# Kernel tuning notes

Hardware: AMD Instinct MI355X
Metric: run time of the kernel (lower is better)

The kernel has to match this reference:

```python
import jax, jax.numpy as jnp
import numpy as np

EPS = 1e-10
LN_EPS = 1e-5
NEG = -1e30
H = 8  # attention_head


def _layernorm(x, g, b):
    mu = jnp.mean(x, axis=-1, keepdims=True)
    var = jnp.mean(jnp.square(x - mu), axis=-1, keepdims=True)
    return (x - mu) * jax.lax.rsqrt(var + LN_EPS) * g + b


def setup_inputs() -> dict:
    key = jax.random.key(0)
    ks = jax.random.split(key, 10)
    B, T, D = 4, 1024, 1024
    inputs = jax.random.normal(ks[0], (B, T, D), dtype=jnp.float32)
    lengths = jax.random.randint(ks[1], (B,), T // 2, T + 1).astype(jnp.int32)
    lengths = lengths.at[0].set(T)  # at least one full-length sequence
    noise_u = jax.random.uniform(ks[2], (B, H, T, T), dtype=jnp.float32)
    w = lambda k: (jax.random.normal(k, (D, D), dtype=jnp.float32) * 0.02)
    return {
        'inputs': inputs, 'lengths': lengths, 'noise_u': noise_u,
        'Wq': w(ks[3]), 'Wk': w(ks[4]), 'Wv': w(ks[5]),
        'Weq': w(ks[6]), 'Wek': w(ks[7]), 'Wfc': w(ks[8]),
        'bfc': jnp.zeros((D,), jnp.float32),
        'ln1_g': jnp.ones((D,), jnp.float32), 'ln1_b': jnp.zeros((D,), jnp.float32),
        'ln2_g': jnp.ones((D,), jnp.float32), 'ln2_b': jnp.zeros((D,), jnp.float32),
    }


def reference(inputs, lengths, noise_u, Wq, Wk, Wv, Weq, Wek, Wfc, bfc,
              ln1_g, ln1_b, ln2_g, ln2_b):
    B, T, D = inputs.shape
    dh = D // H
    # length mask: True where padded
    pad = jnp.arange(T)[None, :] >= lengths[:, None]            # (B, T)
    x = jnp.where(pad[:, :, None], 0.0, inputs)                  # zero padded positions

    def heads(W):
        h = x @ W.T                                              # (B,T,D)
        return h.reshape(B, T, H, dh).transpose(0, 2, 1, 3)      # (B,H,T,dh)

    q, k, v, eq, ek = (heads(W) for W in (Wq, Wk, Wv, Weq, Wek))
    scores = jnp.einsum('bhqd,bhkd->bhqk', q, k) / jnp.sqrt(jnp.float32(D))
    edge = jnp.einsum('bhqd,bhkd->bhqk', eq, ek)                 # (B,H,T,T)

    # bernoulli prior: binary-concrete sample (hard threshold), tau=1
    edges_prob = jax.nn.sigmoid(edge)
    logistic = jnp.log(noise_u + EPS) - jnp.log(1.0 - noise_u + EPS)
    y_soft = jax.nn.sigmoid(jnp.log(edges_prob + EPS) - jnp.log(1.0 - edges_prob + EPS) + logistic)
    gate = y_soft > 0.5                                          # hard edges (condition only, as in torch .data)

    valid = gate & (~pad[:, None, None, :])                      # gate AND key-length mask
    s = jnp.where(valid, scores, NEG)
    attn = jax.nn.softmax(s, axis=-1)
    attn = jnp.where(jnp.any(valid, axis=-1, keepdims=True), attn, 0.0)  # nan->0 for fully-masked rows

    ctx = jax.nn.relu(jnp.einsum('bhqk,bhkd->bhqd', attn, v))
    ctx = ctx.transpose(0, 2, 1, 3).reshape(B, T, D)

    h1 = _layernorm(ctx + x, ln1_g, ln1_b)
    h2 = jax.nn.relu(h1 @ Wfc.T + bfc) + h1
    out = _layernorm(h2, ln2_g, ln2_b)
    out = jnp.where(pad[:, :, None], 0.0, out)
    return out, attn, edges_prob
```

## Files before the change

### kernel.cpp

```cpp
#include <hip/hip_runtime.h>
#include <math.h>

constexpr int Bn = 4, Tn = 1024, Dn = 1024, Hn = 8, DH = 128;
constexpr float EPSF = 1e-10f;
constexpr float LN_EPSF = 1e-5f;
constexpr float NEGF = -1e30f;

typedef __attribute__((ext_vector_type(8))) short bf16x8;
typedef __attribute__((ext_vector_type(4))) float f32x4;
typedef __attribute__((ext_vector_type(4))) unsigned uint4v;

#define MFMA16(a, b, c) __builtin_amdgcn_mfma_f32_16x16x32_bf16(a, b, c, 0, 0, 0)

__device__ __forceinline__ short f2bf(float f) {
    unsigned u = __builtin_bit_cast(unsigned, f);
    u += 0x7fffu + ((u >> 16) & 1u);
    return (short)(u >> 16);
}
__device__ __forceinline__ float bf2f(short h) {
    return __builtin_bit_cast(float, ((unsigned)(unsigned short)h) << 16);
}
__device__ __forceinline__ unsigned pack2(float a, float b) {
    return ((unsigned)(unsigned short)f2bf(a)) | (((unsigned)(unsigned short)f2bf(b)) << 16);
}

__device__ __forceinline__ void gload16(const void* g, void* l) {
    __builtin_amdgcn_global_load_lds((__attribute__((address_space(1))) void*)g,
                                     (__attribute__((address_space(3))) void*)l,
                                     16, 0, 0);
}

template <int NW>
__device__ __forceinline__ void stage_b(const short* g, int ld, short* lds, int lane, int wid) {
#pragma unroll
    for (int s = 0; s < 8 / NW; ++s) {
        const int ii = wid * (8 / NW) + s;
        const int c = ii * 64 + lane;
        const int kb = c >> 7, r = c & 127;
        gload16(g + (size_t)r * ld + kb * 8, lds + ii * 512);
    }
}

template <int NW>
__device__ __forceinline__ void stage_f(const float* g, int ld, float* lds, int lane, int wid) {
#pragma unroll
    for (int s = 0; s < 16 / NW; ++s) {
        const int ii = wid * (16 / NW) + s;
        const int c = ii * 64 + lane;
        const int kb = c >> 8, half = (c >> 7) & 1, r = c & 127;
        gload16(g + (size_t)r * ld + kb * 8 + half * 4, lds + ii * 256);
    }
}

__device__ __forceinline__ bf16x8 fragb(const short* lds, int kbl, int r) {
    return *reinterpret_cast<const bf16x8*>(lds + kbl * 1024 + r * 8);
}

__device__ __forceinline__ bf16x8 fragf(const float* lds, int kbl, int r) {
    const f32x4 lo = *reinterpret_cast<const f32x4*>(lds + kbl * 1024 + r * 4);
    const f32x4 hi = *reinterpret_cast<const f32x4*>(lds + kbl * 1024 + 512 + r * 4);
    uint4v p;
    p[0] = pack2(lo[0], lo[1]);
    p[1] = pack2(lo[2], lo[3]);
    p[2] = pack2(hi[0], hi[1]);
    p[3] = pack2(hi[2], hi[3]);
    return __builtin_bit_cast(bf16x8, p);
}

struct CvtP { const float* src[6]; short* hi; short* lo; };

__global__ __launch_bounds__(256) void cvt_w(CvtP p) {
    const int i = blockIdx.x * 256 + threadIdx.x;
    const int mat = i >> 17;
    const int off = (i & 131071) * 8;
    const float* s = p.src[mat] + off;
    const float4 a = *reinterpret_cast<const float4*>(s);
    const float4 b = *reinterpret_cast<const float4*>(s + 4);
    const float va[8] = {a.x, a.y, a.z, a.w, b.x, b.y, b.z, b.w};
    bf16x8 h, l;
#pragma unroll
    for (int j = 0; j < 8; ++j) {
        h[j] = f2bf(va[j]);
        l[j] = f2bf(va[j] - bf2f(h[j]));
    }
    *reinterpret_cast<bf16x8*>(p.hi + (size_t)mat * 1048576 + off) = h;
    if (mat >= 3)
        *reinterpret_cast<bf16x8*>(p.lo + (size_t)(mat - 3) * 1048576 + off) = l;
}

__global__ __launch_bounds__(256) void mask_x(const float4* __restrict__ in,
                                              const int* __restrict__ lengths,
                                              short* __restrict__ xhi,
                                              short* __restrict__ xlo) {
    const int i = blockIdx.x * 256 + threadIdx.x;
    const int row = i >> 8;
    const int t = row & 1023, b = row >> 10;
    float4 v = in[i];
    if (t >= lengths[b]) { v.x = 0.f; v.y = 0.f; v.z = 0.f; v.w = 0.f; }
    short4 h, l;
    h.x = f2bf(v.x); h.y = f2bf(v.y); h.z = f2bf(v.z); h.w = f2bf(v.w);
    l.x = f2bf(v.x - bf2f(h.x)); l.y = f2bf(v.y - bf2f(h.y));
    l.z = f2bf(v.z - bf2f(h.z)); l.w = f2bf(v.w - bf2f(h.w));
    *reinterpret_cast<short4*>(xhi + (size_t)i * 4) = h;
    *reinterpret_cast<short4*>(xlo + (size_t)i * 4) = l;
}

struct ProjP { const short* whi[5]; const short* wlo[2]; short* o[5]; short* olo[2]; };

__global__ __launch_bounds__(256) void proj_mfma(const short* __restrict__ Xh,
                                                 const short* __restrict__ Xl, ProjP p) {
    __shared__ alignas(16) short T0[4096];
    __shared__ alignas(16) short T1[4096];
    __shared__ alignas(16) short T2[4096];
    __shared__ alignas(16) short T3[4096];
    const int z = blockIdx.z;
    const short* __restrict__ Wh = p.whi[z];
    const int m0 = blockIdx.y << 7, n0 = blockIdx.x << 7;
    const int tid = threadIdx.x, lane = tid & 63, wid = tid >> 6;
    const int wm = (wid >> 1) << 6, wn = (wid & 1) << 6;
    const int kbl = lane >> 4, rl = lane & 15, rw = (lane >> 4) << 2;
    f32x4 acc[4][4] = {};
    if (z < 3) {
        for (int k0 = 0; k0 < Dn; k0 += 32) {
            stage_b<4>(Xh + (size_t)m0 * Dn + k0, Dn, T0, lane, wid);
            stage_b<4>(Wh + (size_t)n0 * Dn + k0, Dn, T1, lane, wid);
            __syncthreads();
            bf16x8 a[4], b[4];
#pragma unroll
            for (int f = 0; f < 4; ++f) {
                a[f] = fragb(T0, kbl, wm + f * 16 + rl);
                b[f] = fragb(T1, kbl, wn + f * 16 + rl);
            }
#pragma unroll
            for (int i = 0; i < 4; ++i)
#pragma unroll
                for (int j = 0; j < 4; ++j)
                    acc[i][j] = MFMA16(a[i], b[j], acc[i][j]);
            __syncthreads();
        }
    } else {
        const short* __restrict__ Wl = p.wlo[z - 3];
        for (int k0 = 0; k0 < Dn; k0 += 32) {
            stage_b<4>(Xh + (size_t)m0 * Dn + k0, Dn, T0, lane, wid);
            stage_b<4>(Xl + (size_t)m0 * Dn + k0, Dn, T1, lane, wid);
            stage_b<4>(Wh + (size_t)n0 * Dn + k0, Dn, T2, lane, wid);
            stage_b<4>(Wl + (size_t)n0 * Dn + k0, Dn, T3, lane, wid);
            __syncthreads();
            bf16x8 ah[4], al[4], bh[4], bl[4];
#pragma unroll
            for (int f = 0; f < 4; ++f) {
                ah[f] = fragb(T0, kbl, wm + f * 16 + rl);
                al[f] = fragb(T1, kbl, wm + f * 16 + rl);
                bh[f] = fragb(T2, kbl, wn + f * 16 + rl);
                bl[f] = fragb(T3, kbl, wn + f * 16 + rl);
            }
#pragma unroll
            for (int i = 0; i < 4; ++i)
#pragma unroll
                for (int j = 0; j < 4; ++j) {
                    acc[i][j] = MFMA16(al[i], bh[j], acc[i][j]);
                    acc[i][j] = MFMA16(ah[i], bl[j], acc[i][j]);
                    acc[i][j] = MFMA16(ah[i], bh[j], acc[i][j]);
                }
            __syncthreads();
        }
    }
    short* __restrict__ O = p.o[z];
    short* __restrict__ OL = (z >= 3) ? p.olo[z - 3] : nullptr;
#pragma unroll
    for (int i = 0; i < 4; ++i)
#pragma unroll
        for (int r = 0; r < 4; ++r) {
            const int m = m0 + wm + i * 16 + rw + r;
            const int b = m >> 10, t = m & 1023;
#pragma unroll
            for (int j = 0; j < 4; ++j) {
                const int n = n0 + wn + j * 16 + rl;
                const int h = n >> 7, d = n & 127;
                const float av = acc[i][j][r];
                if (z == 2) {
                    O[(((size_t)(b * Hn + h) * DH + d) << 10) + t] = f2bf(av);
                } else {
                    const size_t idx = (((size_t)(b * Hn + h)) << 10 | t) * DH + d;
                    const short hi = f2bf(av);
                    O[idx] = hi;
                    if (z >= 3) OL[idx] = f2bf(av - bf2f(hi));
                }
            }
        }
}

__global__ __launch_bounds__(256) void scores_edge(
    const short* __restrict__ Q, const short* __restrict__ Kb,
    const short* __restrict__ EQh, const short* __restrict__ EQl,
    const short* __restrict__ EKh, const short* __restrict__ EKl,
    const float* __restrict__ U, const int* __restrict__ lens,
    float* __restrict__ S, float* __restrict__ EP) {
    __shared__ alignas(16) short T0[4096];
    __shared__ alignas(16) short T1[4096];
    __shared__ alignas(16) short T2[4096];
    __shared__ alignas(16) short T3[4096];
    const int z = blockIdx.z;
    const int len = lens[z >> 3];
    const int m0 = blockIdx.y << 7, n0 = blockIdx.x << 7;
    const int tid = threadIdx.x, lane = tid & 63, wid = tid >> 6;
    const int wm = (wid >> 1) << 6, wn = (wid & 1) << 6;
    const int kbl = lane >> 4, rl = lane & 15, rw = (lane >> 4) << 2;
    const size_t zo = (size_t)z << 17;

    f32x4 acce[4][4] = {};
    for (int k0 = 0; k0 < DH; k0 += 32) {
        stage_b<4>(EQh + zo + (size_t)m0 * DH + k0, DH, T0, lane, wid);
        stage_b<4>(EQl + zo + (size_t)m0 * DH + k0, DH, T1, lane, wid);
        stage_b<4>(EKh + zo + (size_t)n0 * DH + k0, DH, T2, lane, wid);
        stage_b<4>(EKl + zo + (size_t)n0 * DH + k0, DH, T3, lane, wid);
        __syncthreads();
        bf16x8 ah[4], al[4], bh[4], bl[4];
#pragma unroll
        for (int f = 0; f < 4; ++f) {
            ah[f] = fragb(T0, kbl, wm + f * 16 + rl);
            al[f] = fragb(T1, kbl, wm + f * 16 + rl);
            bh[f] = fragb(T2, kbl, wn + f * 16 + rl);
            bl[f] = fragb(T3, kbl, wn + f * 16 + rl);
        }
#pragma unroll
        for (int i = 0; i < 4; ++i)
#pragma unroll
            for (int j = 0; j < 4; ++j) {
                acce[i][j] = MFMA16(al[i], bl[j], acce[i][j]);
                acce[i][j] = MFMA16(al[i], bh[j], acce[i][j]);
                acce[i][j] = MFMA16(ah[i], bl[j], acce[i][j]);
                acce[i][j] = MFMA16(ah[i], bh[j], acce[i][j]);
            }
        __syncthreads();
    }

    f32x4 accs[4][4] = {};
    for (int k0 = 0; k0 < DH; k0 += 32) {
        stage_b<4>(Q + zo + (size_t)m0 * DH + k0, DH, T0, lane, wid);
        stage_b<4>(Kb + zo + (size_t)n0 * DH + k0, DH, T1, lane, wid);
        __syncthreads();
        bf16x8 a[4], b[4];
#pragma unroll
        for (int f = 0; f < 4; ++f) {
            a[f] = fragb(T0, kbl, wm + f * 16 + rl);
            b[f] = fragb(T1, kbl, wn + f * 16 + rl);
        }
#pragma unroll
        for (int i = 0; i < 4; ++i)
#pragma unroll
            for (int j = 0; j < 4; ++j)
                accs[i][j] = MFMA16(a[i], b[j], accs[i][j]);
        __syncthreads();
    }

#pragma unroll
    for (int i = 0; i < 4; ++i)
#pragma unroll
        for (int r = 0; r < 4; ++r) {
            const int m = m0 + wm + i * 16 + rw + r;
#pragma unroll
            for (int j = 0; j < 4; ++j) {
                const int n = n0 + wn + j * 16 + rl;
                const size_t idx = ((size_t)z << 20) + ((size_t)m << 10) + n;
                const float e = acce[i][j][r];
                const float pp = 1.f / (1.f + expf(-e));
                EP[idx] = pp;
                const float u = U[idx];
                const float zz = logf(pp + EPSF) - logf(1.f - pp + EPSF) +
                                 logf(u + EPSF) - logf(1.f - u + EPSF);
                const bool valid = (zz > 0.f) && (n < len);
                S[idx] = valid ? accs[i][j][r] * (1.f / 32.f) : NEGF;
            }
        }
}

__global__ __launch_bounds__(256) void softmax_rows(float* __restrict__ attn) {
    __shared__ float redm[4];
    __shared__ float reds[4];
    const size_t base = (size_t)blockIdx.x * Tn;
    float4* rowp = reinterpret_cast<float4*>(attn + base);
    float4 s = rowp[threadIdx.x];
    float m = fmaxf(fmaxf(s.x, s.y), fmaxf(s.z, s.w));
#pragma unroll
    for (int off = 32; off >= 1; off >>= 1) m = fmaxf(m, __shfl_xor(m, off));
    if ((threadIdx.x & 63) == 0) redm[threadIdx.x >> 6] = m;
    __syncthreads();
    m = fmaxf(fmaxf(redm[0], redm[1]), fmaxf(redm[2], redm[3]));
    const bool any = m > -5e29f;
    float4 e;
    e.x = expf(s.x - m); e.y = expf(s.y - m);
    e.z = expf(s.z - m); e.w = expf(s.w - m);
    float sum = e.x + e.y + e.z + e.w;
#pragma unroll
    for (int off = 32; off >= 1; off >>= 1) sum += __shfl_xor(sum, off);
    if ((threadIdx.x & 63) == 0) reds[threadIdx.x >> 6] = sum;
    __syncthreads();
    sum = reds[0] + reds[1] + reds[2] + reds[3];
    const float inv = any ? 1.f / sum : 0.f;
    e.x *= inv; e.y *= inv; e.z *= inv; e.w *= inv;
    rowp[threadIdx.x] = e;
}

__global__ __launch_bounds__(512) void ctx_mfma(const float* __restrict__ P,
                                                const short* __restrict__ Vt,
                                                float* __restrict__ C) {
    __shared__ alignas(16) float Ps[4096];
    __shared__ alignas(16) short Vs[4096];
    const int z = blockIdx.y;
    const int bb = z >> 3, h = z & 7;
    const int m0 = blockIdx.x << 7;
    const int tid = threadIdx.x, lane = tid & 63, wid = tid >> 6;
    const int wm = (wid >> 2) << 6, wn = (wid & 3) << 5;
    const int kbl = lane >> 4, rl = lane & 15, rw = (lane >> 4) << 2;
    f32x4 acc[4][2] = {};
    for (int k0 = 0; k0 < Tn; k0 += 32) {
        stage_f<8>(P + ((size_t)z << 20) + ((size_t)m0 << 10) + k0, Tn, Ps, lane, wid);
        stage_b<8>(Vt + ((size_t)z << 17) + k0, Tn, Vs, lane, wid);
        __syncthreads();
        bf16x8 a[4], b[2];
#pragma unroll
        for (int f = 0; f < 4; ++f) a[f] = fragf(Ps, kbl, wm + f * 16 + rl);
#pragma unroll
        for (int f = 0; f < 2; ++f) b[f] = fragb(Vs, kbl, wn + f * 16 + rl);
#pragma unroll
        for (int i = 0; i < 4; ++i)
#pragma unroll
            for (int j = 0; j < 2; ++j)
                acc[i][j] = MFMA16(a[i], b[j], acc[i][j]);
        __syncthreads();
    }
#pragma unroll
    for (int i = 0; i < 4; ++i)
#pragma unroll
        for (int r = 0; r < 4; ++r) {
            const int m = m0 + wm + i * 16 + rw + r;
#pragma unroll
            for (int j = 0; j < 2; ++j) {
                const int n = wn + j * 16 + rl;
                C[(((size_t)(bb << 10 | m)) << 10) + h * DH + n] = fmaxf(acc[i][j][r], 0.f);
            }
        }
}

__global__ __launch_bounds__(256) void ln1_kernel(const float* __restrict__ ctx,
                                                  const float* __restrict__ inputs,
                                                  const int* __restrict__ lengths,
                                                  const float* __restrict__ g,
                                                  const float* __restrict__ bb,
                                                  float* __restrict__ h1f,
                                                  short* __restrict__ h1hi,
                                                  short* __restrict__ h1lo) {
    __shared__ float red1[4];
    __shared__ float red2[4];
    const int row = blockIdx.x;
    const int t = row & 1023, b = row >> 10;
    const bool live = t < lengths[b];
    const size_t base = (size_t)row * Dn;
    const int tid = threadIdx.x;
    float4 v = reinterpret_cast<const float4*>(ctx + base)[tid];
    if (live) {
        const float4 r = reinterpret_cast<const float4*>(inputs + base)[tid];
        v.x += r.x; v.y += r.y; v.z += r.z; v.w += r.w;
    }
    float s = v.x + v.y + v.z + v.w;
#pragma unroll
    for (int off = 32; off >= 1; off >>= 1) s += __shfl_xor(s, off);
    if ((tid & 63) == 0) red1[tid >> 6] = s;
    __syncthreads();
    const float mu = (red1[0] + red1[1] + red1[2] + red1[3]) * (1.f / Dn);
    const float d0 = v.x - mu, d1 = v.y - mu, d2 = v.z - mu, d3 = v.w - mu;
    float sq = d0 * d0 + d1 * d1 + d2 * d2 + d3 * d3;
#pragma unroll
    for (int off = 32; off >= 1; off >>= 1) sq += __shfl_xor(sq, off);
    if ((tid & 63) == 0) red2[tid >> 6] = sq;
    __syncthreads();
    const float var = (red2[0] + red2[1] + red2[2] + red2[3]) * (1.f / Dn);
    const float rstd = rsqrtf(var + LN_EPSF);
    const float4 gv = reinterpret_cast<const float4*>(g)[tid];
    const float4 bv = reinterpret_cast<const float4*>(bb)[tid];
    float4 ov;
    ov.x = d0 * rstd * gv.x + bv.x;
    ov.y = d1 * rstd * gv.y + bv.y;
    ov.z = d2 * rstd * gv.z + bv.z;
    ov.w = d3 * rstd * gv.w + bv.w;
    reinterpret_cast<float4*>(h1f + base)[tid] = ov;
    short4 hs, ls;
    hs.x = f2bf(ov.x); hs.y = f2bf(ov.y); hs.z = f2bf(ov.z); hs.w = f2bf(ov.w);
    ls.x = f2bf(ov.x - bf2f(hs.x)); ls.y = f2bf(ov.y - bf2f(hs.y));
    ls.z = f2bf(ov.z - bf2f(hs.z)); ls.w = f2bf(ov.w - bf2f(hs.w));
    reinterpret_cast<short4*>(h1hi + base)[tid] = hs;
    reinterpret_cast<short4*>(h1lo + base)[tid] = ls;
}

__global__ __launch_bounds__(512) void fc_mfma(const short* __restrict__ Xh,
                                               const short* __restrict__ Xl,
                                               const short* __restrict__ Wh,
                                               const short* __restrict__ Wl,
                                               const float* __restrict__ bias,
                                               const float* __restrict__ H1f,
                                               float* __restrict__ O) {
    __shared__ alignas(16) short T0[4096];
    __shared__ alignas(16) short T1[4096];
    __shared__ alignas(16) short T2[4096];
    __shared__ alignas(16) short T3[4096];
    const int m0 = blockIdx.y << 7, n0 = blockIdx.x << 7;
    const int tid = threadIdx.x, lane = tid & 63, wid = tid >> 6;
    const int wm = (wid >> 2) << 6, wn = (wid & 3) << 5;
    const int kbl = lane >> 4, rl = lane & 15, rw = (lane >> 4) << 2;
    f32x4 acc[4][2] = {};
    for (int k0 = 0; k0 < Dn; k0 += 32) {
        stage_b<8>(Xh + (size_t)m0 * Dn + k0, Dn, T0, lane, wid);
        stage_b<8>(Xl + (size_t)m0 * Dn + k0, Dn, T1, lane, wid);
        stage_b<8>(Wh + (size_t)n0 * Dn + k0, Dn, T2, lane, wid);
        stage_b<8>(Wl + (size_t)n0 * Dn + k0, Dn, T3, lane, wid);
        __syncthreads();
        bf16x8 ah[4], al[4], bh[2], bl[2];
#pragma unroll
        for (int f = 0; f < 4; ++f) {
            ah[f] = fragb(T0, kbl, wm + f * 16 + rl);
            al[f] = fragb(T1, kbl, wm + f * 16 + rl);
        }
#pragma unroll
        for (int f = 0; f < 2; ++f) {
            bh[f] = fragb(T2, kbl, wn + f * 16 + rl);
            bl[f] = fragb(T3, kbl, wn + f * 16 + rl);
        }
#pragma unroll
        for (int i = 0; i < 4; ++i)
#pragma unroll
            for (int j = 0; j < 2; ++j) {
                acc[i][j] = MFMA16(al[i], bh[j], acc[i][j]);
                acc[i][j] = MFMA16(ah[i], bl[j], acc[i][j]);
                acc[i][j] = MFMA16(ah[i], bh[j], acc[i][j]);
            }
        __syncthreads();
    }
#pragma unroll
    for (int i = 0; i < 4; ++i)
#pragma unroll
        for (int r = 0; r < 4; ++r) {
            const int m = m0 + wm + i * 16 + rw + r;
#pragma unroll
            for (int j = 0; j < 2; ++j) {
                const int n = n0 + wn + j * 16 + rl;
                const size_t idx = ((size_t)m << 10) + n;
                O[idx] = fmaxf(acc[i][j][r] + bias[n], 0.f) + H1f[idx];
            }
        }
}

__global__ __launch_bounds__(256) void ln2_kernel(const float* __restrict__ a,
                                                  const float* __restrict__ g,
                                                  const float* __restrict__ bb,
                                                  const int* __restrict__ lengths,
                                                  float* __restrict__ o) {
    __shared__ float red1[4];
    __shared__ float red2[4];
    const int row = blockIdx.x;
    const size_t base = (size_t)row * Dn;
    const int tid = threadIdx.x;
    float4 v = reinterpret_cast<const float4*>(a + base)[tid];
    float s = v.x + v.y + v.z + v.w;
#pragma unroll
    for (int off = 32; off >= 1; off >>= 1) s += __shfl_xor(s, off);
    if ((tid & 63) == 0) red1[tid >> 6] = s;
    __syncthreads();
    const float mu = (red1[0] + red1[1] + red1[2] + red1[3]) * (1.f / Dn);
    const float d0 = v.x - mu, d1 = v.y - mu, d2 = v.z - mu, d3 = v.w - mu;
    float sq = d0 * d0 + d1 * d1 + d2 * d2 + d3 * d3;
#pragma unroll
    for (int off = 32; off >= 1; off >>= 1) sq += __shfl_xor(sq, off);
    if ((tid & 63) == 0) red2[tid >> 6] = sq;
    __syncthreads();
    const float var = (red2[0] + red2[1] + red2[2] + red2[3]) * (1.f / Dn);
    const float rstd = rsqrtf(var + LN_EPSF);
    const float4 gv = reinterpret_cast<const float4*>(g)[tid];
    const float4 bv = reinterpret_cast<const float4*>(bb)[tid];
    float4 ov;
    ov.x = d0 * rstd * gv.x + bv.x;
    ov.y = d1 * rstd * gv.y + bv.y;
    ov.z = d2 * rstd * gv.z + bv.z;
    ov.w = d3 * rstd * gv.w + bv.w;
    const int t = row & 1023, b = row >> 10;
    if (t >= lengths[b]) { ov.x = 0.f; ov.y = 0.f; ov.z = 0.f; ov.w = 0.f; }
    reinterpret_cast<float4*>(o + base)[tid] = ov;
}

extern "C" void kernel_launch(void* const* d_in, const int* in_sizes, int n_in,
                              void* d_out, int out_size, void* d_ws, size_t ws_size,
                              hipStream_t stream) {
    const float* inputs = (const float*)d_in[0];
    const int* lengths = (const int*)d_in[1];
    const float* noise = (const float*)d_in[2];
    const float* bfc = (const float*)d_in[9];
    const float* ln1_g = (const float*)d_in[10];
    const float* ln1_b = (const float*)d_in[11];
    const float* ln2_g = (const float*)d_in[12];
    const float* ln2_b = (const float*)d_in[13];

    float* out = (float*)d_out;
    float* attn = out + (size_t)Bn * Tn * Dn;
    float* ep = attn + (size_t)Bn * Hn * Tn * Tn;

    constexpr size_t MB = 1u << 20;
    char* W = (char*)d_ws;
    short* xhi = (short*)(W + 0 * MB);
    short* xlo = (short*)(W + 8 * MB);
    short* whi = (short*)(W + 16 * MB);
    short* wlo = (short*)(W + 28 * MB);
    short* qb = (short*)(W + 34 * MB);
    short* kb = (short*)(W + 42 * MB);
    short* vtb = (short*)(W + 50 * MB);
    short* eqh = (short*)(W + 58 * MB);
    short* eql = (short*)(W + 66 * MB);
    short* ekh = (short*)(W + 74 * MB);
    short* ekl = (short*)(W + 82 * MB);
    float* ctx = (float*)(W + 58 * MB);
    float* h1f = (float*)(W + 74 * MB);
    short* h1hi = (short*)(W + 34 * MB);
    short* h1lo = (short*)(W + 42 * MB);
    float* h2 = (float*)(W + 0 * MB);

    CvtP cp;
    for (int j = 0; j < 6; ++j) cp.src[j] = (const float*)d_in[3 + j];
    cp.hi = whi; cp.lo = wlo;
    cvt_w<<<dim3(3072), 256, 0, stream>>>(cp);

    mask_x<<<dim3(4096), 256, 0, stream>>>((const float4*)inputs, lengths, xhi, xlo);

    ProjP pp;
    for (int j = 0; j < 5; ++j) pp.whi[j] = whi + (size_t)j * 1048576;
    pp.wlo[0] = wlo;
    pp.wlo[1] = wlo + 1048576;
    pp.o[0] = qb; pp.o[1] = kb; pp.o[2] = vtb; pp.o[3] = eqh; pp.o[4] = ekh;
    pp.olo[0] = eql; pp.olo[1] = ekl;
    proj_mfma<<<dim3(8, 32, 5), 256, 0, stream>>>(xhi, xlo, pp);

    scores_edge<<<dim3(8, 8, 32), 256, 0, stream>>>(qb, kb, eqh, eql, ekh, ekl,
                                                    noise, lengths, attn, ep);

    softmax_rows<<<dim3(Bn * Hn * Tn), 256, 0, stream>>>(attn);

    ctx_mfma<<<dim3(8, 32), 512, 0, stream>>>(attn, vtb, ctx);

    ln1_kernel<<<dim3(Bn * Tn), 256, 0, stream>>>(ctx, inputs, lengths, ln1_g, ln1_b,
                                                  h1f, h1hi, h1lo);

    fc_mfma<<<dim3(8, 32), 512, 0, stream>>>(h1hi, h1lo, whi + 5 * 1048576,
                                             wlo + 2 * 1048576, bfc, h1f, h2);

    ln2_kernel<<<dim3(Bn * Tn), 256, 0, stream>>>(h2, ln2_g, ln2_b, lengths, out);
}
```

Measured before the change: 533.5 us.

## Fuse row softmax into ctx matmul kernel and simplify edge gate logit

Removes the standalone softmax kernel and performs an online max/sum softmax over each block's 128 rows at the start of the ctx MFMA kernel, writing normalized probabilities back before the matmul. The gate test now uses the raw edge logit directly instead of recomputing it from the sigmoid via logs, and uses fast exp/log intrinsics. This saves a kernel launch and the separate softmax pass. The fused softmax runs with far fewer blocks and a strided access pattern, which may limit bandwidth, and the simplified gate can differ from the reference near the threshold because EPS terms are dropped.

```diff
diff --git a/kernel.cpp b/kernel.cpp
--- a/kernel.cpp
+++ b/kernel.cpp
@@ -264,53 +264,66 @@
                 const int n = n0 + wn + j * 16 + rl;
                 const size_t idx = ((size_t)z << 20) + ((size_t)m << 10) + n;
                 const float e = acce[i][j][r];
-                const float pp = 1.f / (1.f + expf(-e));
-                EP[idx] = pp;
+                EP[idx] = 1.f / (1.f + __expf(-e));
                 const float u = U[idx];
-                const float zz = logf(pp + EPSF) - logf(1.f - pp + EPSF) +
-                                 logf(u + EPSF) - logf(1.f - u + EPSF);
+                const float zz = e + __logf(u + EPSF) - __logf(1.f - u + EPSF);
                 const bool valid = (zz > 0.f) && (n < len);
                 S[idx] = valid ? accs[i][j][r] * (1.f / 32.f) : NEGF;
             }
         }
 }
 
-__global__ __launch_bounds__(256) void softmax_rows(float* __restrict__ attn) {
-    __shared__ float redm[4];
-    __shared__ float reds[4];
-    const size_t base = (size_t)blockIdx.x * Tn;
-    float4* rowp = reinterpret_cast<float4*>(attn + base);
-    float4 s = rowp[threadIdx.x];
-    float m = fmaxf(fmaxf(s.x, s.y), fmaxf(s.z, s.w));
-#pragma unroll
-    for (int off = 32; off >= 1; off >>= 1) m = fmaxf(m, __shfl_xor(m, off));
-    if ((threadIdx.x & 63) == 0) redm[threadIdx.x >> 6] = m;
-    __syncthreads();
-    m = fmaxf(fmaxf(redm[0], redm[1]), fmaxf(redm[2], redm[3]));
-    const bool any = m > -5e29f;
-    float4 e;
-    e.x = expf(s.x - m); e.y = expf(s.y - m);
-    e.z = expf(s.z - m); e.w = expf(s.w - m);
-    float sum = e.x + e.y + e.z + e.w;
-#pragma unroll
-    for (int off = 32; off >= 1; off >>= 1) sum += __shfl_xor(sum, off);
-    if ((threadIdx.x & 63) == 0) reds[threadIdx.x >> 6] = sum;
-    __syncthreads();
-    sum = reds[0] + reds[1] + reds[2] + reds[3];
-    const float inv = any ? 1.f / sum : 0.f;
-    e.x *= inv; e.y *= inv; e.z *= inv; e.w *= inv;
-    rowp[threadIdx.x] = e;
-}
-
-__global__ __launch_bounds__(512) void ctx_mfma(const float* __restrict__ P,
-                                                const short* __restrict__ Vt,
-                                                float* __restrict__ C) {
+__global__ __launch_bounds__(512) void softmax_ctx(float* __restrict__ P,
+                                                   const short* __restrict__ Vt,
+                                                   float* __restrict__ C) {
     __shared__ alignas(16) float Ps[4096];
     __shared__ alignas(16) short Vs[4096];
     const int z = blockIdx.y;
     const int bb = z >> 3, h = z & 7;
     const int m0 = blockIdx.x << 7;
     const int tid = threadIdx.x, lane = tid & 63, wid = tid >> 6;
+
+    {
+        const int r = tid >> 2, qd = tid & 3;
+        float* rowp = P + ((size_t)z << 20) + ((size_t)(m0 + r) << 10) + qd * 8;
+        float mrun = -3.0e38f, lrun = 0.f;
+#pragma unroll 8
+        for (int c = 0; c < 32; ++c) {
+            const float4 v0 = *reinterpret_cast<const float4*>(rowp + c * 32);
+            const float4 v1 = *reinterpret_cast<const float4*>(rowp + c * 32 + 4);
+            const float cm = fmaxf(fmaxf(fmaxf(v0.x, v0.y), fmaxf(v0.z, v0.w)),
+                                   fmaxf(fmaxf(v1.x, v1.y), fmaxf(v1.z, v1.w)));
+            const float mn = fmaxf(mrun, cm);
+            lrun = lrun * __expf(mrun - mn) +
+                   __expf(v0.x - mn) + __expf(v0.y - mn) +
+                   __expf(v0.z - mn) + __expf(v0.w - mn) +
+                   __expf(v1.x - mn) + __expf(v1.y - mn) +
+                   __expf(v1.z - mn) + __expf(v1.w - mn);
+            mrun = mn;
+        }
+#pragma unroll
+        for (int off = 1; off <= 2; off <<= 1) {
+            const float mo = __shfl_xor(mrun, off);
+            const float lo2 = __shfl_xor(lrun, off);
+            const float mn = fmaxf(mrun, mo);
+            lrun = lrun * __expf(mrun - mn) + lo2 * __expf(mo - mn);
+            mrun = mn;
+        }
+        const float inv = (mrun > -5e29f) ? 1.f / lrun : 0.f;
+#pragma unroll 8
+        for (int c = 0; c < 32; ++c) {
+            float4 v0 = *reinterpret_cast<const float4*>(rowp + c * 32);
+            float4 v1 = *reinterpret_cast<const float4*>(rowp + c * 32 + 4);
+            v0.x = __expf(v0.x - mrun) * inv; v0.y = __expf(v0.y - mrun) * inv;
+            v0.z = __expf(v0.z - mrun) * inv; v0.w = __expf(v0.w - mrun) * inv;
+            v1.x = __expf(v1.x - mrun) * inv; v1.y = __expf(v1.y - mrun) * inv;
+            v1.z = __expf(v1.z - mrun) * inv; v1.w = __expf(v1.w - mrun) * inv;
+            *reinterpret_cast<float4*>(rowp + c * 32) = v0;
+            *reinterpret_cast<float4*>(rowp + c * 32 + 4) = v1;
+        }
+    }
+    __syncthreads();
+
     const int wm = (wid >> 2) << 6, wn = (wid & 3) << 5;
     const int kbl = lane >> 4, rl = lane & 15, rw = (lane >> 4) << 2;
     f32x4 acc[4][2] = {};
@@ -540,9 +553,7 @@
     scores_edge<<<dim3(8, 8, 32), 256, 0, stream>>>(qb, kb, eqh, eql, ekh, ekl,
                                                     noise, lengths, attn, ep);
 
-    softmax_rows<<<dim3(Bn * Hn * Tn), 256, 0, stream>>>(attn);
-
-    ctx_mfma<<<dim3(8, 32), 512, 0, stream>>>(attn, vtb, ctx);
+    softmax_ctx<<<dim3(8, 32), 512, 0, stream>>>(attn, vtb, ctx);
 
     ln1_kernel<<<dim3(Bn * Tn), 256, 0, stream>>>(ctx, inputs, lengths, ln1_g, ln1_b,
                                                   h1f, h1hi, h1lo);
```

After: 516.8 us. -3.1%, faster.
